# Kernel optimization log

Hardware: AMD Instinct MI355X
Metric: run time of the kernel (lower is better)

## Reference

```python
import jax, jax.numpy as jnp
import numpy as np

N_NODES = 81 * 4096   # 4096 graphs x 81 nodes (81 forced by h.view(-1,1,64*81))
N_EDGES = 4_000_000
HID = 32


def _edge_softmax(logits, mask, dst, n):
    # DGL edge_softmax restricted to masked edge subset, normalized per destination node
    NEG = jnp.float32(-1e30)
    l = jnp.where(mask, logits, NEG)
    m = jax.ops.segment_max(l, dst, num_segments=n)
    m = jnp.where(m > -1e29, m, 0.0)  # dst with no masked in-edges
    e = jnp.where(mask, jnp.exp(l - m[dst]), 0.0)
    s = jax.ops.segment_sum(e, dst, num_segments=n)
    return e / jnp.maximum(s[dst], 1e-20)


def _wsgconv(h, src, dst, w, n, W, b, bias, cs, cp, cn):
    pos = w > 0
    neg = w < 0
    a_p = _edge_softmax(w, pos, dst, n)            # softmax of w on positive subgraph
    a_n = _edge_softmax(jnp.abs(w), neg, dst, n)   # softmax of |w| on negative subgraph
    h_p = jax.ops.segment_sum(h[src] * a_p[:, None], dst, num_segments=n)
    h_n = jax.ops.segment_sum(h[src] * a_n[:, None], dst, num_segments=n)
    comb = jnp.concatenate([cs * h, cp * h_p, cn * h_n], axis=1)
    return jax.nn.relu(comb @ W.T + b + bias)


def _conv1d(x, k, stride):
    return jax.lax.conv_general_dilated(x, k, (stride,), 'VALID',
                                        dimension_numbers=('NCH', 'OIH', 'NCH'))


def reference(src, dst, w, n_nodes, W1, b1, bias1, c1s, c1p, c1n,
              W2, b2, bias2, c2s, c2p, c2n, k1, bk1, k2, bk2, Wfc, bfc, Wc, bc):
    n = n_nodes
    deg = jax.ops.segment_sum(jnp.ones_like(w), dst, num_segments=n)
    h0 = deg[:, None]                                  # in_degrees feature [N,1]
    h1 = _wsgconv(h0, src, dst, w, n, W1, b1, bias1, c1s, c1p, c1n)
    h2 = _wsgconv(h1, src, dst, w, n, W2, b2, bias2, c2s, c2p, c2n)
    h = jnp.concatenate([h1, h2], axis=1)              # JumpingKnowledge('cat') -> [N,64]
    # GSAPool(ratio=1.0) returns the input feature unchanged -> identity
    B = n // 81
    x = h.reshape(B, 1, 64 * 81)
    x = _conv1d(x, k1, 64) + bk1[None, :, None]        # [B,16,81]
    x = x[..., :80].reshape(B, 16, 40, 2).max(-1)      # MaxPool1d(2) -> [B,16,40]
    x = _conv1d(x, k2, 3) + bk2[None, :, None]         # [B,32,13]
    x = x.reshape(B, 32 * 13)
    x = jax.nn.relu(x @ Wfc.T + bfc)
    # F.dropout skipped (deterministic reference)
    logits = x @ Wc.T + bc
    return jax.nn.log_softmax(logits, axis=-1)


def setup_inputs():
    key = jax.random.key(0)
    ks = jax.random.split(key, 16)
    s = 0.1
    return {
        'src': jax.random.randint(ks[0], (N_EDGES,), 0, N_NODES),
        'dst': jax.random.randint(ks[1], (N_EDGES,), 0, N_NODES),
        'w': jax.random.normal(ks[2], (N_EDGES,), jnp.float32),
        'n_nodes': N_NODES,
        'W1': jax.random.normal(ks[3], (HID, 3), jnp.float32) * s,
        'b1': jax.random.normal(ks[4], (HID,), jnp.float32) * s,
        'bias1': jnp.zeros((HID,), jnp.float32),
        'c1s': jnp.ones((1,), jnp.float32),
        'c1p': jnp.ones((1,), jnp.float32),
        'c1n': jnp.ones((1,), jnp.float32),
        'W2': jax.random.normal(ks[5], (HID, 3 * HID), jnp.float32) * s,
        'b2': jax.random.normal(ks[6], (HID,), jnp.float32) * s,
        'bias2': jnp.zeros((HID,), jnp.float32),
        'c2s': jnp.ones((1,), jnp.float32),
        'c2p': jnp.ones((1,), jnp.float32),
        'c2n': jnp.ones((1,), jnp.float32),
        'k1': jax.random.normal(ks[7], (16, 1, 64), jnp.float32) * s,
        'bk1': jax.random.normal(ks[8], (16,), jnp.float32) * s,
        'k2': jax.random.normal(ks[9], (32, 16, 3), jnp.float32) * s,
        'bk2': jax.random.normal(ks[10], (32,), jnp.float32) * s,
        'Wfc': jax.random.normal(ks[11], (128, 32 * 13), jnp.float32) * s,
        'bfc': jax.random.normal(ks[12], (128,), jnp.float32) * s,
        'Wc': jax.random.normal(ks[13], (10, 128), jnp.float32) * s,
        'bc': jax.random.normal(ks[14], (10,), jnp.float32) * s,
    }
```

## Files before the change

kernel.cpp:

```cpp
#include <hip/hip_runtime.h>
#include <hip/hip_bf16.h>

#define NNODES 331776
#define NGRAPH 4096
#define NBUCK  2048
#define BNODES 162
#define TE     16384
#define PASSES 4
#define CAP    2560
#define CH     64
#define EB     16

typedef __attribute__((ext_vector_type(8))) short bf8;
typedef __attribute__((ext_vector_type(4))) float f4;
typedef __attribute__((ext_vector_type(4))) unsigned int u32x4;

static __device__ __forceinline__ short f2bf(float x) {
    return (short)__builtin_bit_cast(unsigned short, __float2bfloat16(x));
}
static __device__ __forceinline__ float bf2f(unsigned short u) {
    return __bfloat162float(__hip_bfloat16_raw{u});
}


__global__ __launch_bounds__(256) void k_hist(const int* __restrict__ dst,
                                              int* __restrict__ H, int E) {
    __shared__ int h[NBUCK];
    int t = threadIdx.x, b = blockIdx.x;
    for (int i = t; i < NBUCK; i += 256) h[i] = 0;
    __syncthreads();
    for (int pass = 0; pass < PASSES; pass++) {
        int lo = b * TE + pass * (EB * 256);
        int bins[EB]; bool ok[EB];
#pragma unroll
        for (int i = 0; i < EB; i++) {
            int e = lo + i * 256 + t;
            ok[i] = e < E;
            bins[i] = ok[i] ? (dst[e] / BNODES) : 0;
        }
#pragma unroll
        for (int i = 0; i < EB; i++)
            if (ok[i]) atomicAdd(&h[bins[i]], 1);
    }
    __syncthreads();
    for (int i = t; i < NBUCK; i += 256) H[b * NBUCK + i] = h[i];
}

__global__ __launch_bounds__(256) void k_colA(const int* __restrict__ H,
                                              int* __restrict__ P,
                                              int NT, int CS) {
    int idx = blockIdx.x * 256 + threadIdx.x;
    int bin = idx & (NBUCK - 1);
    int chunk = idx >> 11;
    int t0 = chunk * CS, t1 = min(NT, t0 + CS);
    int s = 0;
    for (int t = t0; t < t1; t++) s += H[t * NBUCK + bin];
    P[chunk * NBUCK + bin] = s;
}

__global__ __launch_bounds__(256) void k_colB(int* __restrict__ P,
                                              int* __restrict__ T) {
    int bin = blockIdx.x * 256 + threadIdx.x;
    int s = 0;
    for (int c = 0; c < CH; c++) {
        int v = P[c * NBUCK + bin];
        P[c * NBUCK + bin] = s;
        s += v;
    }
    T[bin] = s;
}

__global__ __launch_bounds__(256) void k_colC(int* __restrict__ H,
                                              const int* __restrict__ P,
                                              int NT, int CS) {
    int idx = blockIdx.x * 256 + threadIdx.x;
    int bin = idx & (NBUCK - 1);
    int chunk = idx >> 11;
    int t0 = chunk * CS, t1 = min(NT, t0 + CS);
    int s = P[chunk * NBUCK + bin];
    for (int t = t0; t < t1; t++) {
        int v = H[t * NBUCK + bin];
        H[t * NBUCK + bin] = s;
        s += v;
    }
}

__global__ __launch_bounds__(256) void k_binscan(const int* __restrict__ T,
                                                 int* __restrict__ Bstart) {
    __shared__ int tmp[256];
    int t = threadIdx.x;
    int base = t * 8;
    int loc[8]; int s = 0;
#pragma unroll
    for (int i = 0; i < 8; i++) { loc[i] = s; s += T[base + i]; }
    tmp[t] = s; __syncthreads();
    for (int o = 1; o < 256; o <<= 1) {
        int a = (t >= o) ? tmp[t - o] : 0;
        __syncthreads();
        tmp[t] += a;
        __syncthreads();
    }
    int excl = tmp[t] - s;
#pragma unroll
    for (int i = 0; i < 8; i++) Bstart[base + i] = excl + loc[i];
    if (t == 255) Bstart[NBUCK] = excl + s;
}

__global__ __launch_bounds__(256) void k_place(
    const int* __restrict__ src, const int* __restrict__ dst,
    const float* __restrict__ w,
    const int* __restrict__ H, const int* __restrict__ Bstart,
    int2* __restrict__ csrB, int E) {
    __shared__ int cur[NBUCK];
    int t = threadIdx.x, b = blockIdx.x;
    for (int i = t; i < NBUCK; i += 256)
        cur[i] = Bstart[i] + H[b * NBUCK + i];
    __syncthreads();
    for (int pass = 0; pass < PASSES; pass++) {
        int lo = b * TE + pass * (EB * 256);
        int dd[EB], sx[EB]; float wv[EB]; bool ok[EB];
#pragma unroll
        for (int i = 0; i < EB; i++) {
            int e = lo + i * 256 + t;
            ok[i] = e < E;
            if (ok[i]) { dd[i] = dst[e]; sx[i] = src[e]; wv[i] = w[e]; }
        }
        int pk0[EB]; float es[EB]; int bin[EB];
#pragma unroll
        for (int i = 0; i < EB; i++) {
            if (ok[i]) {
                float v = wv[i];
                float e2 = 0.f;
                if (v > 0.f)      e2 = __expf(v);
                else if (v < 0.f) e2 = -__expf(-v);
                es[i] = e2;
                bin[i] = dd[i] / BNODES;
                pk0[i] = sx[i] | ((dd[i] - bin[i] * BNODES) << 19);
            }
        }
        int p[EB];
#pragma unroll
        for (int i = 0; i < EB; i++)
            if (ok[i]) p[i] = atomicAdd(&cur[bin[i]], 1);
#pragma unroll
        for (int i = 0; i < EB; i++)
            if (ok[i]) {
                int2 pk;
                pk.x = pk0[i];
                pk.y = __float_as_int(es[i]);
                csrB[p[i]] = pk;
            }
    }
}

__global__ __launch_bounds__(256) void k_sortbucket(
    int2* __restrict__ csrB, const int* __restrict__ Bstart,
    int* __restrict__ cnt, int* __restrict__ cntp, int* __restrict__ offs) {
    __shared__ int2 pb[CAP];
    __shared__ int lcnt[BNODES * 2];
    __shared__ int lpos[BNODES * 2];
    int t = threadIdx.x, b = blockIdx.x;
    int lo = Bstart[b];
    int S  = Bstart[b + 1] - lo;
    if (S > CAP) S = CAP;
    for (int i = t; i < BNODES * 2; i += 256) lcnt[i] = 0;
    __syncthreads();
    for (int i = t; i < S; i += 256) {
        int2 pk = csrB[lo + i];
        pb[i] = pk;
        int key = ((pk.x >> 19) << 1) | ((unsigned)pk.y >> 31);
        atomicAdd(&lcnt[key], 1);
    }
    __syncthreads();
    if (t == 0) {
        int s = 0;
        for (int i = 0; i < BNODES * 2; i++) { lpos[i] = s; s += lcnt[i]; }
    }
    __syncthreads();
    int node0 = b * BNODES;
    for (int i = t; i < BNODES; i += 256) {
        cnt[node0 + i]  = lcnt[2 * i] + lcnt[2 * i + 1];
        cntp[node0 + i] = lcnt[2 * i];
        offs[node0 + i] = lo + lpos[2 * i];
    }
    __syncthreads();
    for (int i = t; i < S; i += 256) {
        int2 pk = pb[i];
        int local = pk.x >> 19;
        int sign  = (unsigned)pk.y >> 31;
        int key = (local << 1) | sign;
        int p = atomicAdd(&lpos[key], 1);
        int d7 = (node0 + local) & 7;
        int2 outv;
        outv.x = (pk.x & 0x7FFFF) | (d7 << 19) | (sign << 22);
        outv.y = pk.y & 0x7FFFFFFF;
        csrB[lo + p] = outv;
    }
}


__global__ __launch_bounds__(256) void k_layer1(
    const int* __restrict__ cnt, const int* __restrict__ cntp,
    const int* __restrict__ offs, const int2* __restrict__ csr,
    float* __restrict__ spos, float* __restrict__ sneg,
    unsigned short* __restrict__ h1b,
    unsigned long long* __restrict__ xtab,
    const float* __restrict__ W1, const float* __restrict__ b1,
    const float* __restrict__ bias1,
    const float* __restrict__ c1s, const float* __restrict__ c1p,
    const float* __restrict__ c1n) {
    int t = threadIdx.x;
    int g = t >> 5, f = t & 31;
    int d = blockIdx.x * 8 + g;
    int beg = offs[d];
    int len = cnt[d];
    int np  = cntp[d];
    float sp = 0.f, sn = 0.f, up = 0.f, un = 0.f;
    for (int j = 0; j < len; j += 32) {
        int rem = len - j;
        if (f < rem) {
            int2 sw = csr[beg + j + f];
            float es = __int_as_float(sw.y);
            float degs = (float)cnt[sw.x & 0x7FFFF];
            float ep = (j + f < np) ? es : 0.f;
            float en = es - ep;
            sp += ep; sn += en;
            up = fmaf(degs, ep, up); un = fmaf(degs, en, un);
        }
    }
    for (int m = 16; m; m >>= 1) {
        sp += __shfl_xor(sp, m, 32);
        sn += __shfl_xor(sn, m, 32);
        up += __shfl_xor(up, m, 32);
        un += __shfl_xor(un, m, 32);
    }
    if (f == 0) { spos[d] = sp; sneg[d] = sn; }
    float hp = up / fmaxf(sp, 1e-20f);
    float hn = un / fmaxf(sn, 1e-20f);
    float x0 = c1s[0] * (float)len;
    float x1 = c1p[0] * hp;
    float x2 = c1n[0] * hn;
    if (f == 0) {
        unsigned long long u0 = (unsigned short)f2bf(x0);
        unsigned long long u1 = (unsigned short)f2bf(x1);
        unsigned long long u2 = (unsigned short)f2bf(x2);
        xtab[d] = u0 | (u1 << 16) | (u2 << 32) | (0x3F80ULL << 48);
    }
    float v = W1[f * 3] * x0 + W1[f * 3 + 1] * x1 + W1[f * 3 + 2] * x2
            + b1[f] + bias1[f];
    v = fmaxf(v, 0.f);
    h1b[d * 32 + f] = (unsigned short)f2bf(v);
}


__global__ __launch_bounds__(256) void k_agg(
    const int* __restrict__ cnt, const int* __restrict__ offs,
    const int2* __restrict__ csr,
    const float* __restrict__ spos, const float* __restrict__ sneg,
    const unsigned long long* __restrict__ xtab,
    const unsigned short* __restrict__ W1Tb,
    unsigned short* __restrict__ hpb, unsigned short* __restrict__ hnb,
    int E) {
    __shared__ unsigned short Hl[4][32][40];
    int t = threadIdx.x;
    int wv = t >> 6, lane = t & 63;
    int col = lane & 15, quad = lane >> 4;
    int d0 = (blockIdx.x * 4 + wv) * 8;
    int beg = offs[d0];
    int totlen = 0;
#pragma unroll
    for (int i = 0; i < 8; i++) totlen += cnt[d0 + i];

    bf8 B1[2];
#pragma unroll
    for (int fh = 0; fh < 2; fh++) {
        u32x4 bw = {0u, 0u, 0u, 0u};
        if (quad == 0) {
            int n = fh * 16 + col;
            unsigned w0 = W1Tb[0 * 32 + n], w1 = W1Tb[1 * 32 + n];
            unsigned w2 = W1Tb[2 * 32 + n], w3 = W1Tb[3 * 32 + n];
            bw.x = w0 | (w1 << 16);
            bw.y = w2 | (w3 << 16);
        }
        B1[fh] = __builtin_bit_cast(bf8, bw);
    }

    f4 acc2[2] = {{0.f, 0.f, 0.f, 0.f}, {0.f, 0.f, 0.f, 0.f}};
    unsigned short (*myH)[40] = Hl[wv];
    int nw = (totlen + 31) >> 5;

    for (int w = 0; w < nw; w++) {
        int eidx = w * 32 + (lane & 31);
        bool val = eidx < totlen;
        int gidx = beg + (val ? eidx : 0);
        long long rec = *(const long long*)(csr + gidx);
        int x = (int)rec;
        float ef = __int_as_float((int)(rec >> 32));
        int slot = val ? (((x >> 19) & 7) * 2 + ((x >> 22) & 1)) : 255;
        unsigned es16 = (unsigned)(unsigned short)f2bf(ef);
        int pk = (int)(es16 | ((unsigned)slot << 16));

#pragma unroll
        for (int eh = 0; eh < 2; eh++) {
            int xm = __builtin_amdgcn_ds_bpermute((eh * 16 + col) * 4, x);
            unsigned srcn = (unsigned)xm & 0x7FFFF;
            unsigned long long r8 = 0;
            if (quad == 0) r8 = xtab[srcn];
            u32x4 av = {(unsigned)r8, (unsigned)(r8 >> 32), 0u, 0u};
            bf8 A1 = __builtin_bit_cast(bf8, av);
#pragma unroll
            for (int fh = 0; fh < 2; fh++) {
                f4 h = {0.f, 0.f, 0.f, 0.f};
                h = __builtin_amdgcn_mfma_f32_16x16x32_bf16(A1, B1[fh], h, 0, 0, 0);
#pragma unroll
                for (int i = 0; i < 4; i += 2) {
                    float lo = fmaxf(h[i], 0.f), hi = fmaxf(h[i + 1], 0.f);
                    unsigned u;
                    asm("v_cvt_pk_bf16_f32 %0, %1, %2" : "=v"(u) : "v"(lo), "v"(hi));
                    *(unsigned*)&myH[fh * 16 + col][eh * 16 + quad * 4 + i] = u;
                }
            }
        }

        unsigned aw[4];
#pragma unroll
        for (int j2 = 0; j2 < 4; j2++) {
            int k0 = quad * 8 + j2 * 2;
            int p0 = __builtin_amdgcn_ds_bpermute(k0 * 4, pk);
            int p1 = __builtin_amdgcn_ds_bpermute((k0 + 1) * 4, pk);
            unsigned e0 = (((unsigned)p0 >> 16) == (unsigned)col)
                        ? ((unsigned)p0 & 0xFFFFu) : 0u;
            unsigned e1 = (((unsigned)p1 >> 16) == (unsigned)col)
                        ? ((unsigned)p1 & 0xFFFFu) : 0u;
            aw[j2] = e0 | (e1 << 16);
        }
        bf8 A2 = __builtin_bit_cast(bf8, (u32x4){aw[0], aw[1], aw[2], aw[3]});

#pragma unroll
        for (int fh = 0; fh < 2; fh++) {
            bf8 B2 = *(const bf8*)&myH[fh * 16 + col][quad * 8];
            acc2[fh] = __builtin_amdgcn_mfma_f32_16x16x32_bf16(A2, B2, acc2[fh], 0, 0, 0);
        }
    }

#pragma unroll
    for (int i = 0; i < 4; i++) {
        int slot = quad * 4 + i;
        int node = d0 + (slot >> 1);
        float s = (slot & 1) ? sneg[node] : spos[node];
        float r = 1.0f / fmaxf(s, 1e-20f);
        unsigned short* bp = (slot & 1) ? hnb : hpb;
#pragma unroll
        for (int fh = 0; fh < 2; fh++) {
            float v = acc2[fh][i] * r;
            bp[(size_t)node * 32 + fh * 16 + col] = (unsigned short)f2bf(v);
        }
    }
}


__global__ __launch_bounds__(256) void k_prep(
    const float* __restrict__ W2, const float* __restrict__ c2s,
    const float* __restrict__ c2p, const float* __restrict__ c2n,
    const float* __restrict__ k1,
    const float* __restrict__ W1, const float* __restrict__ b1,
    const float* __restrict__ bias1,
    unsigned short* __restrict__ W2sT, unsigned short* __restrict__ k1T,
    unsigned short* __restrict__ W1Tb) {
    int i = blockIdx.x * 256 + threadIdx.x;
    if (i < 96 * 32) {
        int k = i >> 5, n = i & 31;
        float sc = (k < 32) ? c2s[0] : ((k < 64) ? c2p[0] : c2n[0]);
        W2sT[i] = (unsigned short)f2bf(W2[n * 96 + k] * sc);
    } else if (i < 96 * 32 + 64 * 16) {
        int j = i - 3072;
        int k = j >> 4, o = j & 15;
        k1T[j] = (unsigned short)f2bf(k1[o * 64 + k]);
    } else if (i < 96 * 32 + 64 * 16 + 4 * 32) {
        int j = i - (3072 + 1024);
        int k = j >> 5, n = j & 31;
        float v = (k < 3) ? W1[n * 3 + k] : (b1[n] + bias1[n]);
        W1Tb[j] = (unsigned short)f2bf(v);
    }
}


__global__ __launch_bounds__(256) void k_mlp_mfma(
    const unsigned short* __restrict__ h1b,
    const unsigned short* __restrict__ hpb, const unsigned short* __restrict__ hnb,
    const unsigned short* __restrict__ W2sT, const unsigned short* __restrict__ k1T,
    const float* __restrict__ b2, const float* __restrict__ bias2,
    const float* __restrict__ bk1,
    float* __restrict__ y1) {
    __shared__ unsigned short h2s[4][16 * 32];
    int t = threadIdx.x;
    int wv = t >> 6;
    int lane = t & 63;
    int col = lane & 15;
    int quad = lane >> 4;

    float bv0 = b2[col] + bias2[col];
    float bv1 = b2[col + 16] + bias2[col + 16];
    float bky = bk1[col];

    bf8 BW[2][3];
#pragma unroll
    for (int nt = 0; nt < 2; nt++)
#pragma unroll
        for (int kt = 0; kt < 3; kt++) {
            bf8 b;
#pragma unroll
            for (int j = 0; j < 8; j++)
                b[j] = (short)W2sT[(kt * 32 + quad * 8 + j) * 32 + nt * 16 + col];
            BW[nt][kt] = b;
        }
    bf8 BK[2];
#pragma unroll
    for (int kt = 0; kt < 2; kt++) {
        bf8 b;
#pragma unroll
        for (int j = 0; j < 8; j++)
            b[j] = (short)k1T[(kt * 32 + quad * 8 + j) * 16 + col];
        BK[kt] = b;
    }
    unsigned short* myT = h2s[wv];

#pragma unroll 1
    for (int g = 0; g < 4; g++) {
        int nbase = blockIdx.x * 256 + wv * 64 + g * 16;
        int node = nbase + col;
        bf8 a0 = *(const bf8*)(h1b + (size_t)node * 32 + quad * 8);
        bf8 a1 = *(const bf8*)(hpb + (size_t)node * 32 + quad * 8);
        bf8 a2 = *(const bf8*)(hnb + (size_t)node * 32 + quad * 8);

        f4 acc0 = {bv0, bv0, bv0, bv0};
        f4 acc1 = {bv1, bv1, bv1, bv1};
        acc0 = __builtin_amdgcn_mfma_f32_16x16x32_bf16(a0, BW[0][0], acc0, 0, 0, 0);
        acc0 = __builtin_amdgcn_mfma_f32_16x16x32_bf16(a1, BW[0][1], acc0, 0, 0, 0);
        acc0 = __builtin_amdgcn_mfma_f32_16x16x32_bf16(a2, BW[0][2], acc0, 0, 0, 0);
        acc1 = __builtin_amdgcn_mfma_f32_16x16x32_bf16(a0, BW[1][0], acc1, 0, 0, 0);
        acc1 = __builtin_amdgcn_mfma_f32_16x16x32_bf16(a1, BW[1][1], acc1, 0, 0, 0);
        acc1 = __builtin_amdgcn_mfma_f32_16x16x32_bf16(a2, BW[1][2], acc1, 0, 0, 0);

#pragma unroll
        for (int i = 0; i < 4; i++) {
            int r = quad * 4 + i;
            myT[r * 32 + col]      = (unsigned short)f2bf(fmaxf(acc0[i], 0.f));
            myT[r * 32 + col + 16] = (unsigned short)f2bf(fmaxf(acc1[i], 0.f));
        }
        bf8 ah2 = *(const bf8*)(myT + col * 32 + quad * 8);

        f4 accy = {bky, bky, bky, bky};
        accy = __builtin_amdgcn_mfma_f32_16x16x32_bf16(a0,  BK[0], accy, 0, 0, 0);
        accy = __builtin_amdgcn_mfma_f32_16x16x32_bf16(ah2, BK[1], accy, 0, 0, 0);
#pragma unroll
        for (int i = 0; i < 4; i++)
            y1[(size_t)(nbase + quad * 4 + i) * 16 + col] = accy[i];
    }
}


__global__ void k_transpose(const float* __restrict__ Wfc, float* __restrict__ WfcT) {
    int i = blockIdx.x * 256 + threadIdx.x;
    if (i < 128 * 416) {
        int u = i / 416, c = i - u * 416;
        WfcT[c * 128 + u] = Wfc[i];
    }
}


__global__ __launch_bounds__(256) void k_head(
    const float* __restrict__ y1, const float* __restrict__ k2,
    const float* __restrict__ bk2, const float* __restrict__ WfcT,
    const float* __restrict__ bfc, const float* __restrict__ Wc,
    const float* __restrict__ bc, float* __restrict__ out) {
    __shared__ float yl[1296];
    __shared__ float zl[16][41];
    __shared__ float xr[416];
    __shared__ float k2s[1536];
    __shared__ float fl2[256];
    __shared__ float fl[128];
    __shared__ float ll[10];
    int t = threadIdx.x;
    int b = blockIdx.x;
    const float4* yb4 = (const float4*)(y1 + (size_t)b * 1296);
    for (int i = t; i < 324; i += 256) ((float4*)yl)[i] = yb4[i];
    for (int i = t; i < 1536; i += 256) k2s[i] = k2[i];
    __syncthreads();
    for (int i = t; i < 640; i += 256) {
        int ic = i & 15, p = i >> 4;
        zl[ic][p] = fmaxf(yl[(2 * p) * 16 + ic], yl[(2 * p + 1) * 16 + ic]);
    }
    __syncthreads();
    for (int i = t; i < 416; i += 256) {
        int oc = i / 13, tt = i - oc * 13;
        float acc = bk2[oc];
        for (int ic = 0; ic < 16; ic++) {
            const float* kk = &k2s[(oc * 16 + ic) * 3];
            acc += zl[ic][3 * tt]     * kk[0]
                 + zl[ic][3 * tt + 1] * kk[1]
                 + zl[ic][3 * tt + 2] * kk[2];
        }
        xr[i] = acc;
    }
    __syncthreads();
    {
        int u = t & 127, q = t >> 7;
        float acc = 0.f;
        for (int i = q * 208; i < q * 208 + 208; i++)
            acc = fmaf(xr[i], WfcT[i * 128 + u], acc);
        fl2[t] = acc;
    }
    __syncthreads();
    if (t < 128)
        fl[t] = fmaxf(fl2[t] + fl2[t + 128] + bfc[t], 0.f);
    __syncthreads();
    if (t < 160) {
        int c = t >> 4, l = t & 15;
        float acc = 0.f;
        for (int i = l * 8; i < l * 8 + 8; i++)
            acc += fl[i] * Wc[c * 128 + i];
        for (int m = 8; m; m >>= 1) acc += __shfl_down(acc, m, 16);
        if (l == 0) ll[c] = acc + bc[c];
    }
    __syncthreads();
    if (t < 10) {
        float m = -1e30f;
        for (int c = 0; c < 10; c++) m = fmaxf(m, ll[c]);
        float s = 0.f;
        for (int c = 0; c < 10; c++) s += __expf(ll[c] - m);
        out[b * 10 + t] = ll[t] - m - __logf(s);
    }
}


extern "C" void kernel_launch(void* const* d_in, const int* in_sizes, int n_in,
                              void* d_out, int out_size, void* d_ws, size_t ws_size,
                              hipStream_t stream) {
    const int*   src   = (const int*)d_in[0];
    const int*   dst   = (const int*)d_in[1];
    const float* w     = (const float*)d_in[2];
    const float* W1    = (const float*)d_in[4];
    const float* b1    = (const float*)d_in[5];
    const float* bias1 = (const float*)d_in[6];
    const float* c1s   = (const float*)d_in[7];
    const float* c1p   = (const float*)d_in[8];
    const float* c1n   = (const float*)d_in[9];
    const float* W2    = (const float*)d_in[10];
    const float* b2    = (const float*)d_in[11];
    const float* bias2 = (const float*)d_in[12];
    const float* c2s   = (const float*)d_in[13];
    const float* c2p   = (const float*)d_in[14];
    const float* c2n   = (const float*)d_in[15];
    const float* k1    = (const float*)d_in[16];
    const float* bk1   = (const float*)d_in[17];
    const float* k2    = (const float*)d_in[18];
    const float* bk2   = (const float*)d_in[19];
    const float* Wfc   = (const float*)d_in[20];
    const float* bfc   = (const float*)d_in[21];
    const float* Wc    = (const float*)d_in[22];
    const float* bc    = (const float*)d_in[23];
    const int E = in_sizes[0];
    const int NT = (E + TE - 1) / TE;
    const int CS = (NT + CH - 1) / CH;

    size_t off = 0;
    auto carve = [&](size_t bytes) -> char* {
        char* p = (char*)d_ws + off;
        off = (off + bytes + 255) & ~(size_t)255;
        return p;
    };
    int*   cnt    = (int*)  carve((size_t)NNODES * 4);
    int*   cntp   = (int*)  carve((size_t)NNODES * 4);
    int*   offs   = (int*)  carve((size_t)NNODES * 4);
    int2*  csrB   = (int2*) carve((size_t)E * 8);
    int*   H      = (int*)  carve((size_t)NT * NBUCK * 4);
    int*   P      = (int*)  carve((size_t)CH * NBUCK * 4);
    int*   T      = (int*)  carve((size_t)NBUCK * 4);
    int*   Bstart = (int*)  carve((size_t)(NBUCK + 1) * 4);
    float* spos   = (float*)carve((size_t)NNODES * 4);
    float* sneg   = (float*)carve((size_t)NNODES * 4);
    unsigned short* h1b = (unsigned short*)carve((size_t)NNODES * 32 * 2);
    unsigned short* hpb = (unsigned short*)carve((size_t)NNODES * 32 * 2);
    unsigned short* hnb = (unsigned short*)carve((size_t)NNODES * 32 * 2);
    float* y1     = (float*)carve((size_t)NNODES * 16 * 4);
    float* WfcT   = (float*)carve((size_t)128 * 416 * 4);
    unsigned short* W2sT = (unsigned short*)carve((size_t)96 * 32 * 2);
    unsigned short* k1T  = (unsigned short*)carve((size_t)64 * 16 * 2);
    unsigned short* W1Tb = (unsigned short*)carve((size_t)4 * 32 * 2);
    unsigned long long* xtab = (unsigned long long*)y1;
    (void)ws_size;

    k_hist      <<<NT, 256, 0, stream>>>(dst, H, E);
    k_colA      <<<CH * NBUCK / 256, 256, 0, stream>>>(H, P, NT, CS);
    k_colB      <<<NBUCK / 256, 256, 0, stream>>>(P, T);
    k_colC      <<<CH * NBUCK / 256, 256, 0, stream>>>(H, P, NT, CS);
    k_binscan   <<<1, 256, 0, stream>>>(T, Bstart);
    k_place     <<<NT, 256, 0, stream>>>(src, dst, w, H, Bstart, csrB, E);
    k_sortbucket<<<NBUCK, 256, 0, stream>>>(csrB, Bstart, cnt, cntp, offs);
    k_layer1    <<<NNODES / 8, 256, 0, stream>>>(cnt, cntp, offs, csrB,
                                                 spos, sneg, h1b, xtab,
                                                 W1, b1, bias1, c1s, c1p, c1n);
    k_prep      <<<17, 256, 0, stream>>>(W2, c2s, c2p, c2n, k1,
                                         W1, b1, bias1, W2sT, k1T, W1Tb);
    k_transpose <<<(128 * 416 + 255) / 256, 256, 0, stream>>>(Wfc, WfcT);
    k_agg       <<<NNODES / 32, 256, 0, stream>>>(cnt, offs, csrB,
                                                  spos, sneg, xtab, W1Tb,
                                                  hpb, hnb, E);
    k_mlp_mfma  <<<NNODES / 256, 256, 0, stream>>>(h1b, hpb, hnb, W2sT, k1T,
                                                   b2, bias2, bk1, y1);
    k_head      <<<NGRAPH, 256, 0, stream>>>(y1, k2, bk2, WfcT, bfc, Wc, bc,
                                             (float*)d_out);
}
```

Baseline: 402.6 us.

## Stage bucket scatter through shared memory for coalesced global writes in k_place

New measurement: 380.0 us. 5.6% less time.

```diff
diff --git a/kernel.cpp b/kernel.cpp
--- a/kernel.cpp
+++ b/kernel.cpp
@@ -106,50 +106,94 @@
     if (t == 255) Bstart[NBUCK] = excl + s;
 }
 
-__global__ __launch_bounds__(256) void k_place(
+__global__ __launch_bounds__(1024) void k_place(
     const int* __restrict__ src, const int* __restrict__ dst,
     const float* __restrict__ w,
     const int* __restrict__ H, const int* __restrict__ Bstart,
     int2* __restrict__ csrB, int E) {
-    __shared__ int cur[NBUCK];
+    __shared__ int2 pb[TE];
+    __shared__ int lstart[NBUCK + 1];
+    __shared__ int gshift[NBUCK];
+    __shared__ int lcur[NBUCK];
+    __shared__ int tsum[1024];
     int t = threadIdx.x, b = blockIdx.x;
-    for (int i = t; i < NBUCK; i += 256)
-        cur[i] = Bstart[i] + H[b * NBUCK + i];
-    __syncthreads();
-    for (int pass = 0; pass < PASSES; pass++) {
-        int lo = b * TE + pass * (EB * 256);
-        int dd[EB], sx[EB]; float wv[EB]; bool ok[EB];
-#pragma unroll
-        for (int i = 0; i < EB; i++) {
-            int e = lo + i * 256 + t;
-            ok[i] = e < E;
-            if (ok[i]) { dd[i] = dst[e]; sx[i] = src[e]; wv[i] = w[e]; }
-        }
-        int pk0[EB]; float es[EB]; int bin[EB];
-#pragma unroll
-        for (int i = 0; i < EB; i++) {
-            if (ok[i]) {
-                float v = wv[i];
+    for (int i = t; i < NBUCK; i += 1024) lcur[i] = 0;
+    __syncthreads();
+    {
+        int bins[16];
+#pragma unroll
+        for (int k = 0; k < 16; k++) {
+            int e = b * TE + k * 1024 + t;
+            bins[k] = (e < E) ? (dst[e] / BNODES) : -1;
+        }
+#pragma unroll
+        for (int k = 0; k < 16; k++)
+            if (bins[k] >= 0) atomicAdd(&lcur[bins[k]], 1);
+    }
+    __syncthreads();
+    int b0 = t * 2;
+    int c0 = lcur[b0], c1 = lcur[b0 + 1];
+    tsum[t] = c0 + c1;
+    __syncthreads();
+    for (int o = 1; o < 1024; o <<= 1) {
+        int a = (t >= o) ? tsum[t - o] : 0;
+        __syncthreads();
+        tsum[t] += a;
+        __syncthreads();
+    }
+    int excl = tsum[t] - (c0 + c1);
+    lstart[b0] = excl;
+    lstart[b0 + 1] = excl + c0;
+    if (t == 1023) lstart[NBUCK] = excl + c0 + c1;
+    gshift[b0]     = Bstart[b0]     + H[b * NBUCK + b0]     - excl;
+    gshift[b0 + 1] = Bstart[b0 + 1] + H[b * NBUCK + b0 + 1] - (excl + c0);
+    lcur[b0] = excl;
+    lcur[b0 + 1] = excl + c0;
+    __syncthreads();
+    {
+        int dd[16], sx[16]; float wv[16]; bool ok[16];
+#pragma unroll
+        for (int k = 0; k < 16; k++) {
+            int e = b * TE + k * 1024 + t;
+            ok[k] = e < E;
+            if (ok[k]) { dd[k] = dst[e]; sx[k] = src[e]; wv[k] = w[e]; }
+        }
+        int pk0[16]; float es[16]; int bin[16];
+#pragma unroll
+        for (int k = 0; k < 16; k++) {
+            if (ok[k]) {
+                float v = wv[k];
                 float e2 = 0.f;
                 if (v > 0.f)      e2 = __expf(v);
                 else if (v < 0.f) e2 = -__expf(-v);
-                es[i] = e2;
-                bin[i] = dd[i] / BNODES;
-                pk0[i] = sx[i] | ((dd[i] - bin[i] * BNODES) << 19);
+                es[k] = e2;
+                bin[k] = dd[k] / BNODES;
+                pk0[k] = sx[k] | ((dd[k] - bin[k] * BNODES) << 19);
             }
         }
-        int p[EB];
-#pragma unroll
-        for (int i = 0; i < EB; i++)
-            if (ok[i]) p[i] = atomicAdd(&cur[bin[i]], 1);
-#pragma unroll
-        for (int i = 0; i < EB; i++)
-            if (ok[i]) {
-                int2 pk;
-                pk.x = pk0[i];
-                pk.y = __float_as_int(es[i]);
-                csrB[p[i]] = pk;
+        int p[16];
+#pragma unroll
+        for (int k = 0; k < 16; k++)
+            if (ok[k]) p[k] = atomicAdd(&lcur[bin[k]], 1);
+#pragma unroll
+        for (int k = 0; k < 16; k++)
+            if (ok[k]) {
+                int2 pk; pk.x = pk0[k]; pk.y = __float_as_int(es[k]);
+                pb[p[k]] = pk;
             }
+    }
+    __syncthreads();
+    int S = lstart[NBUCK];
+    for (int k = 0; k < 16; k++) {
+        int i = k * 1024 + t;
+        if (i < S) {
+            int lo = 0, hi = NBUCK;
+            while (hi - lo > 1) {
+                int mid = (lo + hi) >> 1;
+                if (lstart[mid] <= i) lo = mid; else hi = mid;
+            }
+            csrB[gshift[lo] + i] = pb[i];
+        }
     }
 }
 
@@ -596,7 +640,7 @@
     k_colB      <<<NBUCK / 256, 256, 0, stream>>>(P, T);
     k_colC      <<<CH * NBUCK / 256, 256, 0, stream>>>(H, P, NT, CS);
     k_binscan   <<<1, 256, 0, stream>>>(T, Bstart);
-    k_place     <<<NT, 256, 0, stream>>>(src, dst, w, H, Bstart, csrB, E);
+    k_place     <<<NT, 1024, 0, stream>>>(src, dst, w, H, Bstart, csrB, E);
     k_sortbucket<<<NBUCK, 256, 0, stream>>>(csrB, Bstart, cnt, cntp, offs);
     k_layer1    <<<NNODES / 8, 256, 0, stream>>>(cnt, cntp, offs, csrB,
                                                  spos, sneg, h1b, xtab,
```
